# Kernel tuning notes

Measured on AMD Instinct MI355X. Metric: run time of the kernel, lower is better.

## Reference

```python
import jax, jax.numpy as jnp
import numpy as np

NUM_STEPS = 32
THRESHOLD = 1.0
SLOPE = 25.0  # snntorch fast_sigmoid default slope

@jax.custom_vjp
def spike_fn(x):
    # Heaviside forward, fast-sigmoid surrogate backward
    return (x > 0).astype(x.dtype)

def _spike_fwd(x):
    return spike_fn(x), x

def _spike_bwd(x, g):
    return (g / (SLOPE * jnp.abs(x) + 1.0) ** 2,)

spike_fn.defvjp(_spike_fwd, _spike_bwd)


def setup_inputs() -> dict:
    key = jax.random.key(0)
    ks = jax.random.split(key, 4)
    B, F, H, O = 2048, 768, 1024, 16
    def w(k, shape, fan_in):
        return jax.random.normal(k, shape, jnp.float32) / np.float32(np.sqrt(fan_in))
    return {
        "fused": jax.random.normal(ks[0], (B, F), jnp.float32),
        "W_in": w(ks[1], (F, H), F),
        "b_in": jnp.zeros((H,), jnp.float32),
        "W_rec": w(ks[2], (H, H), H),
        "b_rec": jnp.zeros((H,), jnp.float32),
        "W_out": w(ks[3], (H, O), H),
        "b_out": jnp.zeros((O,), jnp.float32),
        "resonant_decay": jnp.full((H,), 0.6, jnp.float32),
        "resonant_frequency": jnp.full((H,), 0.2, jnp.float32),
    }


def reference(fused, W_in, b_in, W_rec, b_rec, W_out, b_out,
              resonant_decay, resonant_frequency):
    # base_current = fusion_in(fused): [B, H]
    base = fused @ W_in + b_in
    decay = 0.55 + 0.4 * jax.nn.sigmoid(resonant_decay)       # [H]
    freq = 0.1 + 0.9 * jax.nn.sigmoid(resonant_frequency)     # [H]
    z = jnp.zeros_like(base)

    def step(carry, _):
        membrane, resonance, recurrent_current = carry
        drive = base + recurrent_current
        resonance = decay * resonance + freq * membrane
        membrane = decay * membrane + drive - resonance
        spikes = spike_fn(membrane - THRESHOLD)
        membrane = membrane - spikes * THRESHOLD
        recurrent_current = spikes @ W_rec + b_rec
        return (membrane, resonance, recurrent_current), spikes

    _, spike_trace = jax.lax.scan(step, (z, z, z), None, length=NUM_STEPS)
    # spike_trace: [T, B, H] (torch stacks on dim=1, mean over time is identical)
    pooled = spike_trace.mean(axis=0)                          # [B, H]
    output = pooled @ W_out + b_out                            # [B, O]
    return output
```

## Files before the change

### kernel.cpp

```cpp
#include <hip/hip_runtime.h>

typedef __attribute__((ext_vector_type(4))) float f32x4;
typedef __attribute__((ext_vector_type(4))) int   i32x4;
typedef __attribute__((ext_vector_type(8))) short s16x8;

#define MFMA16(a, b, c)  __builtin_amdgcn_mfma_f32_16x16x32_bf16((a), (b), (c), 0, 0, 0)
#define MFMAI8(a, b, c)  __builtin_amdgcn_mfma_i32_16x16x64_i8((a), (b), (c), 0, 0, 0)

#define QINV (1.0f / 252.0f)

typedef __attribute__((address_space(3))) unsigned int lds_uint;
typedef const __attribute__((address_space(1))) unsigned int glob_uint;
__device__ __forceinline__ void glds16(const void* g, void* l) {
    __builtin_amdgcn_global_load_lds((glob_uint*)g, (lds_uint*)l, 16, 0, 0);
}

#define SBARL()                                                                \
    {                                                                          \
        __builtin_amdgcn_sched_barrier(0);                                     \
        asm volatile("s_waitcnt lgkmcnt(0)" ::: "memory");                     \
        __builtin_amdgcn_s_barrier();                                          \
        __builtin_amdgcn_sched_barrier(0);                                     \
    }
#define SBAR()                                                                 \
    {                                                                          \
        __builtin_amdgcn_sched_barrier(0);                                     \
        __builtin_amdgcn_s_barrier();                                          \
        __builtin_amdgcn_sched_barrier(0);                                     \
    }

__device__ inline unsigned short f2bf(float f) {
    unsigned int u = __float_as_uint(f);
    return (unsigned short)((u + 0x7FFFu + ((u >> 16) & 1u)) >> 16);
}
__device__ inline float bf2f(unsigned short b) {
    return __uint_as_float(((unsigned int)b) << 16);
}

__global__ __launch_bounds__(256) void k_pack3(const float* __restrict__ W,
                                               unsigned short* __restrict__ L1,
                                               unsigned short* __restrict__ L2,
                                               unsigned short* __restrict__ L3,
                                               int K) {
    int idx = blockIdx.x * 256 + threadIdx.x;
    if (idx >= K * 1024) return;
    int k = idx >> 10;
    int n = idx & 1023;
    float x = W[idx];
    unsigned short h1 = f2bf(x);  float r1 = x - bf2f(h1);
    unsigned short h2 = f2bf(r1); float r2 = r1 - bf2f(h2);
    unsigned short h3 = f2bf(r2);
    size_t o = ((size_t)(k >> 5) << 15) + ((size_t)n << 5) + (k & 31);
    L1[o] = h1; L2[o] = h2; L3[o] = h3;
}

__global__ __launch_bounds__(256) void k_colmax(const float* __restrict__ W,
                                                float* __restrict__ t1) {
    __shared__ float red[256];
    int n = blockIdx.x;
    float m = 0.f;
    for (int k = threadIdx.x; k < 1024; k += 256)
        m = fmaxf(m, fabsf(W[(size_t)k * 1024 + n]));
    red[threadIdx.x] = m;
    __syncthreads();
    for (int s = 128; s > 0; s >>= 1) {
        if (threadIdx.x < s) red[threadIdx.x] = fmaxf(red[threadIdx.x], red[threadIdx.x + s]);
        __syncthreads();
    }
    if (threadIdx.x == 0) t1[n] = fmaxf(red[0], 1e-30f) * (1.0f / 126.0f);
}

__global__ __launch_bounds__(256) void k_packq(const float* __restrict__ W,
                                               const float* __restrict__ t1a,
                                               signed char* __restrict__ Q) {
    int idx = blockIdx.x * 256 + threadIdx.x;
    int k = idx >> 10;
    int n = idx & 1023;
    float x = W[idx];
    float T1 = t1a[n];
    float T2 = T1 * QINV;
    float T3 = T2 * QINV;
    float q1 = rintf(x / T1);  float r1 = fmaf(-q1, T1, x);
    float q2 = rintf(r1 / T2); float r2 = fmaf(-q2, T2, r1);
    float q3 = rintf(r2 / T3);
    int kt = k >> 6, cg = n >> 4;
    int lane = (((k >> 4) & 3) << 4) | (n & 15);
    size_t base = ((size_t)((kt * 64 + cg) * 3)) << 10;
    size_t lj = (size_t)lane * 16 + (k & 15);
    Q[base + lj]        = (signed char)(int)q1;
    Q[base + 1024 + lj] = (signed char)(int)q2;
    Q[base + 2048 + lj] = (signed char)(int)q3;
}

#define FSTR 770
#define LDS_SPK    0
#define LDS_DEC    32768
#define LDS_FRQ    33792
#define LDS_T1     34816
#define LDS_RING   35840
#define LDS_FUSED  35840
#define LDS_PLDS   35840
#define LDS_TOTAL  134400

#define RING_NT(P, nt, BSRC)                                                   \
    {                                                                          \
        asm volatile("s_waitcnt vmcnt(9)" ::: "memory");                       \
        __builtin_amdgcn_sched_barrier(0);                                     \
        const char* sl = ring + (P) + (nt) * 3072;                             \
        i32x4 Bv0 = *(const i32x4*)(sl + lane16);                              \
        i32x4 Bv1 = *(const i32x4*)(sl + 1024 + lane16);                       \
        i32x4 Bv2 = *(const i32x4*)(sl + 2048 + lane16);                       \
        acc[0][nt][0] = MFMAI8(Af0, Bv0, acc[0][nt][0]);                       \
        acc[1][nt][0] = MFMAI8(Af1, Bv0, acc[1][nt][0]);                       \
        acc[0][nt][1] = MFMAI8(Af0, Bv1, acc[0][nt][1]);                       \
        acc[1][nt][1] = MFMAI8(Af1, Bv1, acc[1][nt][1]);                       \
        acc[0][nt][2] = MFMAI8(Af0, Bv2, acc[0][nt][2]);                       \
        acc[1][nt][2] = MFMAI8(Af1, Bv2, acc[1][nt][2]);                       \
        __builtin_amdgcn_sched_barrier(0);                                     \
        glds16((BSRC),        (void*)sl);                                      \
        glds16((BSRC) + 1024, (void*)(sl + 1024));                             \
        glds16((BSRC) + 2048, (void*)(sl + 2048));                             \
    }
#define RING_NTL(P, nt, N)                                                     \
    {                                                                          \
        asm volatile("s_waitcnt vmcnt(" #N ")" ::: "memory");                  \
        __builtin_amdgcn_sched_barrier(0);                                     \
        const char* sl = ring + (P) + (nt) * 3072;                             \
        i32x4 Bv0 = *(const i32x4*)(sl + lane16);                              \
        i32x4 Bv1 = *(const i32x4*)(sl + 1024 + lane16);                       \
        i32x4 Bv2 = *(const i32x4*)(sl + 2048 + lane16);                       \
        acc[0][nt][0] = MFMAI8(Af0, Bv0, acc[0][nt][0]);                       \
        acc[1][nt][0] = MFMAI8(Af1, Bv0, acc[1][nt][0]);                       \
        acc[0][nt][1] = MFMAI8(Af0, Bv1, acc[0][nt][1]);                       \
        acc[1][nt][1] = MFMAI8(Af1, Bv1, acc[1][nt][1]);                       \
        acc[0][nt][2] = MFMAI8(Af0, Bv2, acc[0][nt][2]);                       \
        acc[1][nt][2] = MFMAI8(Af1, Bv2, acc[1][nt][2]);                       \
    }

__global__ __launch_bounds__(512, 2) void k_main(const float* __restrict__ fused,
                                                 const unsigned short* __restrict__ Wi1,
                                                 const unsigned short* __restrict__ Wi2,
                                                 const unsigned short* __restrict__ Wi3,
                                                 const float* __restrict__ b_in,
                                                 const signed char* __restrict__ WrQ,
                                                 const float* __restrict__ t1a,
                                                 const float* __restrict__ b_rec,
                                                 const float* __restrict__ rdec,
                                                 const float* __restrict__ rfrq,
                                                 const float* __restrict__ W_out,
                                                 const float* __restrict__ b_out,
                                                 char* __restrict__ sx,
                                                 unsigned long long* __restrict__ pdb,
                                                 unsigned int* __restrict__ flags,
                                                 float* __restrict__ out) {
    extern __shared__ __align__(16) char smem[];
    const int tid = threadIdx.x;
    const int w = tid >> 6, lane = tid & 63;
    const int llo = lane & 15, lhi = lane >> 4;
    const int bid = blockIdx.x;
    const int q = bid >> 2, h = bid & 3;
    const int r0 = q * 32;
    const int cbase = h * 256;
    const int cg0 = h * 16 + w * 2;
    const int lane16 = lane * 16;
    const int ax = (llo & 7) << 4;

    float* fl = (float*)(smem + LDS_FUSED);
    for (int i = tid; i < 32 * 768; i += 512) {
        int rr = i / 768, cc = i - rr * 768;
        fl[rr * FSTR + cc] = fused[(size_t)(r0 + rr) * 768 + cc];
    }
    __syncthreads();

    f32x4 bacc[2][2] = {};
    for (int kt = 0; kt < 24; ++kt) {
        s16x8 a1v[2], a2v[2], a3v[2];
#pragma unroll
        for (int m = 0; m < 2; ++m) {
            const float* ap = fl + (m * 16 + llo) * FSTR + kt * 32 + lhi * 8;
#pragma unroll
            for (int j = 0; j < 8; ++j) {
                float x = ap[j];
                unsigned short h1 = f2bf(x);  float r1 = x - bf2f(h1);
                unsigned short h2 = f2bf(r1); float r2 = r1 - bf2f(h2);
                a1v[m][j] = (short)h1; a2v[m][j] = (short)h2; a3v[m][j] = (short)f2bf(r2);
            }
        }
#pragma unroll
        for (int nt = 0; nt < 2; ++nt) {
            int c = cbase + w * 32 + nt * 16 + llo;
            size_t boff = ((size_t)(kt * 1024 + c) << 5) + lhi * 8;
            s16x8 b1 = *(const s16x8*)&Wi1[boff];
            s16x8 b2 = *(const s16x8*)&Wi2[boff];
            s16x8 b3 = *(const s16x8*)&Wi3[boff];
#pragma unroll
            for (int m = 0; m < 2; ++m) {
                bacc[m][nt] = MFMA16(a1v[m], b1, bacc[m][nt]);
                bacc[m][nt] = MFMA16(a1v[m], b2, bacc[m][nt]);
                bacc[m][nt] = MFMA16(a2v[m], b1, bacc[m][nt]);
                bacc[m][nt] = MFMA16(a2v[m], b2, bacc[m][nt]);
                bacc[m][nt] = MFMA16(a1v[m], b3, bacc[m][nt]);
                bacc[m][nt] = MFMA16(a3v[m], b1, bacc[m][nt]);
            }
        }
    }
    __syncthreads();

    float* ldsDec = (float*)(smem + LDS_DEC);
    float* ldsFrq = (float*)(smem + LDS_FRQ);
    float* ldsT1  = (float*)(smem + LDS_T1);
    if (tid < 256) {
        int c = cbase + tid;
        ldsDec[tid] = (float)(0.55 + 0.4 / (1.0 + exp(-(double)rdec[c])));
        ldsFrq[tid] = (float)(0.10 + 0.9 / (1.0 + exp(-(double)rfrq[c])));
        ldsT1[tid]  = t1a[c];
    }

    float base2[2][2][4];
    float mem[2][2][4], res[2][2][4];
    unsigned int pooled_pk[4] = {0, 0, 0, 0};
    char* ring = smem + LDS_RING + w * 12288;
    unsigned long long myb = 0;
#pragma unroll
    for (int m = 0; m < 2; ++m)
#pragma unroll
        for (int nt = 0; nt < 2; ++nt) {
            int c = cbase + w * 32 + nt * 16 + llo;
            float bb = b_in[c];
            float brv = b_rec[c];
#pragma unroll
            for (int fr = 0; fr < 4; ++fr) {
                int row = m * 16 + lhi * 4 + fr;
                float b0 = __fadd_rn(bacc[m][nt][fr], bb);
                base2[m][nt][fr] = __fadd_rn(b0, brv);
                float m_ = __fadd_rn(0.f, b0);
                int s = (m_ > 1.0f) ? 1 : 0;
                res[m][nt][fr] = 0.f;
                mem[m][nt][fr] = __fadd_rn(m_, -(float)s);
                pooled_pk[m * 2 + nt] += (unsigned int)s << (8 * fr);
                unsigned long long b = __ballot(s);
                myb = (lane == (m * 8 + nt * 4 + fr)) ? b : myb;
                *(unsigned char*)(smem + ((row * 1024 + c) ^ ((row & 7) << 4))) =
                    (unsigned char)s;
            }
        }
    if (lane < 16)
        __hip_atomic_store((unsigned long long*)(sx + q * 4096 + h * 1024 + w * 128 + lane * 8),
                           myb, __ATOMIC_RELAXED, __HIP_MEMORY_SCOPE_AGENT);
    __builtin_amdgcn_sched_barrier(0);
    {
#pragma unroll
        for (int kk = 0; kk < 2; ++kk)
#pragma unroll
            for (int nt = 0; nt < 2; ++nt) {
                const signed char* b =
                    WrQ + (((size_t)(((4 * h + kk) * 64 + cg0 + nt) * 3)) << 10) + lane16;
                char* sl = ring + kk * 6144 + nt * 3072;
                glds16(b,        (void*)sl);
                glds16(b + 1024, (void*)(sl + 1024));
                glds16(b + 2048, (void*)(sl + 2048));
            }
    }
    __builtin_amdgcn_sched_barrier(0);
    asm volatile("s_waitcnt vmcnt(12)" ::: "memory");
    SBARL();
    if (tid == 0)
        __hip_atomic_store(&flags[q * 4 + h], 1u,
                           __ATOMIC_RELAXED, __HIP_MEMORY_SCOPE_AGENT);

    for (int t = 1; t < 32; ++t) {
        i32x4 acc[2][2][3] = {};

#pragma unroll
        for (int i = 0; i < 4; ++i) {
            const int kt = 4 * h + i;
            const int P = (i & 1) * 6144;
            i32x4 Af0 = *(const i32x4*)(smem + ((llo * 1024 + kt * 64 + lhi * 16) ^ ax));
            i32x4 Af1 = *(const i32x4*)(smem + (((16 + llo) * 1024 + kt * 64 + lhi * 16) ^ ax));
            const int nkt = (kt + 2) & 15;
            const signed char* b0 = WrQ + (((size_t)((nkt * 64 + cg0) * 3)) << 10) + lane16;
            const signed char* b1 = WrQ + (((size_t)((nkt * 64 + cg0 + 1) * 3)) << 10) + lane16;
            RING_NT(P, 0, b0)
            RING_NT(P, 1, b1)
        }

        if (tid < 4 && tid != h) {
            while (__hip_atomic_load(&flags[(t - 1) * 256 + q * 4 + tid],
                                     __ATOMIC_ACQUIRE, __HIP_MEMORY_SCOPE_AGENT) == 0)
                __builtin_amdgcn_s_sleep(2);
        }
        SBAR();
        if (tid < 384) {
            int hh = tid >> 7;
            int hsrc = hh + (hh >= h ? 1 : 0);
            int inner = tid & 127;
            unsigned long long B = __hip_atomic_load(
                (unsigned long long*)(sx + (((t - 1) & 1) * 262144) + q * 4096
                                      + hsrc * 1024 + inner * 8),
                __ATOMIC_RELAXED, __HIP_MEMORY_SCOPE_AGENT);
            int l = inner & 15, wsrc = inner >> 4;
            int fr = l & 3, nt = (l >> 2) & 1, m = (l >> 3) & 1;
            int colb = hsrc * 256 + wsrc * 32 + nt * 16;
#pragma unroll
            for (int l2 = 0; l2 < 4; ++l2) {
                int row = m * 16 + l2 * 4 + fr;
                unsigned int b16 = (unsigned int)(B >> (l2 * 16)) & 0xFFFFu;
                i32x4 v;
#pragma unroll
                for (int qq = 0; qq < 4; ++qq) {
                    unsigned int b4 = (b16 >> (qq * 4)) & 0xFu;
                    v[qq] = (int)((b4 & 1u) | ((b4 >> 1) & 1u) << 8 |
                                  ((b4 >> 2) & 1u) << 16 | ((b4 >> 3) & 1u) << 24);
                }
                *(i32x4*)(smem + ((row * 1024 + colb) ^ ((row & 7) << 4))) = v;
            }
        }
        SBARL();

#pragma unroll 2
        for (int i = 4; i < 14; ++i) {
            const int kt = (4 * h + i) & 15;
            const int P = (i & 1) * 6144;
            i32x4 Af0 = *(const i32x4*)(smem + ((llo * 1024 + kt * 64 + lhi * 16) ^ ax));
            i32x4 Af1 = *(const i32x4*)(smem + (((16 + llo) * 1024 + kt * 64 + lhi * 16) ^ ax));
            const int nkt = (4 * h + i + 2) & 15;
            const signed char* b0 = WrQ + (((size_t)((nkt * 64 + cg0) * 3)) << 10) + lane16;
            const signed char* b1 = WrQ + (((size_t)((nkt * 64 + cg0 + 1) * 3)) << 10) + lane16;
            RING_NT(P, 0, b0)
            RING_NT(P, 1, b1)
        }
        {
            const int kt = (4 * h + 14) & 15;
            i32x4 Af0 = *(const i32x4*)(smem + ((llo * 1024 + kt * 64 + lhi * 16) ^ ax));
            i32x4 Af1 = *(const i32x4*)(smem + (((16 + llo) * 1024 + kt * 64 + lhi * 16) ^ ax));
            RING_NTL(0, 0, 9) RING_NTL(0, 1, 6)
        }
        {
            const int kt = (4 * h + 15) & 15;
            i32x4 Af0 = *(const i32x4*)(smem + ((llo * 1024 + kt * 64 + lhi * 16) ^ ax));
            i32x4 Af1 = *(const i32x4*)(smem + (((16 + llo) * 1024 + kt * 64 + lhi * 16) ^ ax));
            RING_NTL(6144, 0, 3) RING_NTL(6144, 1, 0)
        }

        myb = 0;
#pragma unroll
        for (int m = 0; m < 2; ++m)
#pragma unroll
            for (int nt = 0; nt < 2; ++nt) {
                int lc = w * 32 + nt * 16 + llo;
                int c = cbase + lc;
                float dcc = ldsDec[lc], fqc = ldsFrq[lc], t1c = ldsT1[lc];
#pragma unroll
                for (int fr = 0; fr < 4; ++fr) {
                    int row = m * 16 + lhi * 4 + fr;
                    float s3 = (float)acc[m][nt][2][fr];
                    float s2 = fmaf(s3, QINV, (float)acc[m][nt][1][fr]);
                    float rec = __fmul_rn(fmaf(s2, QINV, (float)acc[m][nt][0][fr]), t1c);
                    float drive = __fadd_rn(base2[m][nt][fr], rec);
                    float rnew = __fadd_rn(__fmul_rn(dcc, res[m][nt][fr]),
                                           __fmul_rn(fqc, mem[m][nt][fr]));
                    float tt = __fadd_rn(__fmul_rn(dcc, mem[m][nt][fr]), drive);
                    float m_ = __fadd_rn(tt, -rnew);
                    int s = (m_ > 1.0f) ? 1 : 0;
                    res[m][nt][fr] = rnew;
                    mem[m][nt][fr] = __fadd_rn(m_, -(float)s);
                    pooled_pk[m * 2 + nt] += (unsigned int)s << (8 * fr);
                    unsigned long long b = __ballot(s);
                    myb = (lane == (m * 8 + nt * 4 + fr)) ? b : myb;
                    if (t < 31)
                        *(unsigned char*)(smem + ((row * 1024 + c) ^ ((row & 7) << 4))) =
                            (unsigned char)s;
                }
            }
        if (t < 31) {
            if (lane < 16)
                __hip_atomic_store((unsigned long long*)(sx + ((t & 1) * 262144) + q * 4096
                                                         + h * 1024 + w * 128 + lane * 8),
                                   myb, __ATOMIC_RELAXED, __HIP_MEMORY_SCOPE_AGENT);
            __builtin_amdgcn_sched_barrier(0);
#pragma unroll
            for (int kk = 0; kk < 2; ++kk)
#pragma unroll
                for (int nt = 0; nt < 2; ++nt) {
                    const signed char* b =
                        WrQ + (((size_t)(((4 * h + kk) * 64 + cg0 + nt) * 3)) << 10) + lane16;
                    char* sl = ring + kk * 6144 + nt * 3072;
                    glds16(b,        (void*)sl);
                    glds16(b + 1024, (void*)(sl + 1024));
                    glds16(b + 2048, (void*)(sl + 2048));
                }
            __builtin_amdgcn_sched_barrier(0);
            asm volatile("s_waitcnt vmcnt(12)" ::: "memory");
            SBARL();
            if (tid == 0)
                __hip_atomic_store(&flags[t * 256 + q * 4 + h], 1u,
                                   __ATOMIC_RELAXED, __HIP_MEMORY_SCOPE_AGENT);
        }
    }

    __syncthreads();
    float* plds = (float*)(smem + LDS_PLDS);
#pragma unroll
    for (int m = 0; m < 2; ++m)
#pragma unroll
        for (int nt = 0; nt < 2; ++nt) {
            int lc = w * 32 + nt * 16 + llo;
#pragma unroll
            for (int fr = 0; fr < 4; ++fr)
                plds[(m * 16 + lhi * 4 + fr) * 264 + lc] =
                    (float)((pooled_pk[m * 2 + nt] >> (8 * fr)) & 255u) * 0.03125f;
        }
    __syncthreads();
    double part = 0.0;
    {
        int row = tid >> 4, o = tid & 15;
        for (int j = 0; j < 256; ++j)
            part += (double)plds[row * 264 + j] * (double)W_out[(size_t)(cbase + j) * 16 + o];
    }
    if (h != 0) {
        __hip_atomic_store(&pdb[(q * 4 + h) * 512 + tid], __double_as_longlong(part),
                           __ATOMIC_RELAXED, __HIP_MEMORY_SCOPE_AGENT);
        __syncthreads();
        if (tid == 0)
            __hip_atomic_store(&flags[32 * 256 + q * 4 + h], 1u,
                               __ATOMIC_RELEASE, __HIP_MEMORY_SCOPE_AGENT);
    } else {
        if (tid == 0) {
#pragma unroll
            for (int hp = 1; hp < 4; ++hp)
                while (__hip_atomic_load(&flags[32 * 256 + q * 4 + hp],
                                         __ATOMIC_ACQUIRE, __HIP_MEMORY_SCOPE_AGENT) == 0)
                    __builtin_amdgcn_s_sleep(2);
        }
        __syncthreads();
        {
            int row = tid >> 4, o = tid & 15;
            double tot = part;
#pragma unroll
            for (int hp = 1; hp < 4; ++hp) {
                unsigned long long pb = __hip_atomic_load(&pdb[(q * 4 + hp) * 512 + tid],
                                                          __ATOMIC_RELAXED,
                                                          __HIP_MEMORY_SCOPE_AGENT);
                tot += __longlong_as_double(pb);
            }
            out[(size_t)(r0 + row) * 16 + o] = __fadd_rn((float)tot, b_out[o]);
        }
    }
}

extern "C" void kernel_launch(void* const* d_in, const int* in_sizes, int n_in,
                              void* d_out, int out_size, void* d_ws, size_t ws_size,
                              hipStream_t stream) {
    const float* fused = (const float*)d_in[0];
    const float* W_in  = (const float*)d_in[1];
    const float* b_in  = (const float*)d_in[2];
    const float* W_rec = (const float*)d_in[3];
    const float* b_rec = (const float*)d_in[4];
    const float* W_out = (const float*)d_in[5];
    const float* b_out = (const float*)d_in[6];
    const float* rdec  = (const float*)d_in[7];
    const float* rfrq  = (const float*)d_in[8];

    char* ws = (char*)d_ws;
    signed char*        WrQ   = (signed char*)(ws);
    float*              t1a   = (float*)(ws + 3145728);
    unsigned short*     Wi1   = (unsigned short*)(ws + 3407872);
    unsigned short*     Wi2   = (unsigned short*)(ws + 4980736);
    unsigned short*     Wi3   = (unsigned short*)(ws + 6553600);
    char*               sx    = ws + 8126464;
    unsigned long long* pdb   = (unsigned long long*)(ws + 8650752);
    unsigned int*       flags = (unsigned int*)(ws + 9699328);
    float* out = (float*)d_out;

    hipFuncSetAttribute((const void*)k_main,
                        hipFuncAttributeMaxDynamicSharedMemorySize, LDS_TOTAL);

    hipMemsetAsync(flags, 0, 33 * 256 * 4, stream);
    hipLaunchKernelGGL(k_colmax, dim3(1024), dim3(256), 0, stream, W_rec, t1a);
    hipLaunchKernelGGL(k_packq, dim3(4096), dim3(256), 0, stream, W_rec, t1a, WrQ);
    hipLaunchKernelGGL(k_pack3, dim3(3072), dim3(256), 0, stream, W_in, Wi1, Wi2, Wi3, 768);

    void* args[] = {(void*)&fused, (void*)&Wi1, (void*)&Wi2, (void*)&Wi3, (void*)&b_in,
                    (void*)&WrQ, (void*)&t1a, (void*)&b_rec, (void*)&rdec, (void*)&rfrq,
                    (void*)&W_out, (void*)&b_out, (void*)&sx, (void*)&pdb, (void*)&flags,
                    (void*)&out};
    hipLaunchCooperativeKernel((void*)k_main, dim3(256), dim3(512), args, LDS_TOTAL, stream);
}
```

Baseline: 444.9 us.

## Overlap per-thread flag polling with MFMA work and coalesce column-max reduction

The main loop no longer has a single thread per source poll the flags followed by a block barrier. Each of the 384 loader threads now spins on its own source's flag and loads the spike bits right away, with two of the four local k-tiles of MFMA work placed between the poll and the unpack so the wait overlaps compute. Separately, the column-max prepass now reads W_rec row-coalesced across 128 blocks and merges results with an integer atomicMax. That needs an extra memset, and packq now writes the final scale. The trade is many more spinning threads and extra atomics in exchange for removing one barrier and the strided loads.

```diff
diff --git a/kernel.cpp b/kernel.cpp
--- a/kernel.cpp
+++ b/kernel.cpp
@@ -19,12 +19,6 @@
     {                                                                          \
         __builtin_amdgcn_sched_barrier(0);                                     \
         asm volatile("s_waitcnt lgkmcnt(0)" ::: "memory");                     \
-        __builtin_amdgcn_s_barrier();                                          \
-        __builtin_amdgcn_sched_barrier(0);                                     \
-    }
-#define SBAR()                                                                 \
-    {                                                                          \
-        __builtin_amdgcn_sched_barrier(0);                                     \
         __builtin_amdgcn_s_barrier();                                          \
         __builtin_amdgcn_sched_barrier(0);                                     \
     }
@@ -55,29 +49,29 @@
 }
 
 __global__ __launch_bounds__(256) void k_colmax(const float* __restrict__ W,
-                                                float* __restrict__ t1) {
-    __shared__ float red[256];
-    int n = blockIdx.x;
-    float m = 0.f;
-    for (int k = threadIdx.x; k < 1024; k += 256)
-        m = fmaxf(m, fabsf(W[(size_t)k * 1024 + n]));
-    red[threadIdx.x] = m;
-    __syncthreads();
-    for (int s = 128; s > 0; s >>= 1) {
-        if (threadIdx.x < s) red[threadIdx.x] = fmaxf(red[threadIdx.x], red[threadIdx.x + s]);
-        __syncthreads();
-    }
-    if (threadIdx.x == 0) t1[n] = fmaxf(red[0], 1e-30f) * (1.0f / 126.0f);
+                                                unsigned int* __restrict__ t1u) {
+    __shared__ float cmax[1024];
+    for (int i = threadIdx.x; i < 1024; i += 256) cmax[i] = 0.f;
+    __syncthreads();
+    int k0 = blockIdx.x * 8;
+    for (int r = 0; r < 8; ++r)
+        for (int c = threadIdx.x; c < 1024; c += 256)
+            cmax[c] = fmaxf(cmax[c], fabsf(W[(size_t)(k0 + r) * 1024 + c]));
+    __syncthreads();
+    for (int c = threadIdx.x; c < 1024; c += 256)
+        atomicMax(&t1u[c], __float_as_uint(cmax[c]));
 }
 
 __global__ __launch_bounds__(256) void k_packq(const float* __restrict__ W,
-                                               const float* __restrict__ t1a,
+                                               const unsigned int* __restrict__ t1u,
+                                               float* __restrict__ t1a,
                                                signed char* __restrict__ Q) {
     int idx = blockIdx.x * 256 + threadIdx.x;
     int k = idx >> 10;
     int n = idx & 1023;
     float x = W[idx];
-    float T1 = t1a[n];
+    float T1 = fmaxf(__uint_as_float(t1u[n]), 1e-30f) * (1.0f / 126.0f);
+    if (k == 0) t1a[n] = T1;
     float T2 = T1 * QINV;
     float T3 = T2 * QINV;
     float q1 = rintf(x / T1);  float r1 = fmaf(-q1, T1, x);
@@ -272,7 +266,7 @@
         i32x4 acc[2][2][3] = {};
 
 #pragma unroll
-        for (int i = 0; i < 4; ++i) {
+        for (int i = 0; i < 2; ++i) {
             const int kt = 4 * h + i;
             const int P = (i & 1) * 6144;
             i32x4 Af0 = *(const i32x4*)(smem + ((llo * 1024 + kt * 64 + lhi * 16) ^ ax));
@@ -284,27 +278,42 @@
             RING_NT(P, 1, b1)
         }
 
-        if (tid < 4 && tid != h) {
-            while (__hip_atomic_load(&flags[(t - 1) * 256 + q * 4 + tid],
+        unsigned long long Bbits = 0;
+        int hsrc_t = 0, inner_t = 0;
+        if (tid < 384) {
+            int hh = tid >> 7;
+            hsrc_t = hh + (hh >= h ? 1 : 0);
+            inner_t = tid & 127;
+            while (__hip_atomic_load(&flags[(t - 1) * 256 + q * 4 + hsrc_t],
                                      __ATOMIC_ACQUIRE, __HIP_MEMORY_SCOPE_AGENT) == 0)
                 __builtin_amdgcn_s_sleep(2);
-        }
-        SBAR();
+            Bbits = __hip_atomic_load(
+                (unsigned long long*)(sx + (((t - 1) & 1) * 262144) + q * 4096
+                                      + hsrc_t * 1024 + inner_t * 8),
+                __ATOMIC_RELAXED, __HIP_MEMORY_SCOPE_AGENT);
+        }
+
+#pragma unroll
+        for (int i = 2; i < 4; ++i) {
+            const int kt = 4 * h + i;
+            const int P = (i & 1) * 6144;
+            i32x4 Af0 = *(const i32x4*)(smem + ((llo * 1024 + kt * 64 + lhi * 16) ^ ax));
+            i32x4 Af1 = *(const i32x4*)(smem + (((16 + llo) * 1024 + kt * 64 + lhi * 16) ^ ax));
+            const int nkt = (kt + 2) & 15;
+            const signed char* b0 = WrQ + (((size_t)((nkt * 64 + cg0) * 3)) << 10) + lane16;
+            const signed char* b1 = WrQ + (((size_t)((nkt * 64 + cg0 + 1) * 3)) << 10) + lane16;
+            RING_NT(P, 0, b0)
+            RING_NT(P, 1, b1)
+        }
+
         if (tid < 384) {
-            int hh = tid >> 7;
-            int hsrc = hh + (hh >= h ? 1 : 0);
-            int inner = tid & 127;
-            unsigned long long B = __hip_atomic_load(
-                (unsigned long long*)(sx + (((t - 1) & 1) * 262144) + q * 4096
-                                      + hsrc * 1024 + inner * 8),
-                __ATOMIC_RELAXED, __HIP_MEMORY_SCOPE_AGENT);
-            int l = inner & 15, wsrc = inner >> 4;
+            int l = inner_t & 15, wsrc = inner_t >> 4;
             int fr = l & 3, nt = (l >> 2) & 1, m = (l >> 3) & 1;
-            int colb = hsrc * 256 + wsrc * 32 + nt * 16;
+            int colb = hsrc_t * 256 + wsrc * 32 + nt * 16;
 #pragma unroll
             for (int l2 = 0; l2 < 4; ++l2) {
                 int row = m * 16 + l2 * 4 + fr;
-                unsigned int b16 = (unsigned int)(B >> (l2 * 16)) & 0xFFFFu;
+                unsigned int b16 = (unsigned int)(Bbits >> (l2 * 16)) & 0xFFFFu;
                 i32x4 v;
 #pragma unroll
                 for (int qq = 0; qq < 4; ++qq) {
@@ -464,6 +473,7 @@
     char* ws = (char*)d_ws;
     signed char*        WrQ   = (signed char*)(ws);
     float*              t1a   = (float*)(ws + 3145728);
+    unsigned int*       t1u   = (unsigned int*)(ws + 3149824);
     unsigned short*     Wi1   = (unsigned short*)(ws + 3407872);
     unsigned short*     Wi2   = (unsigned short*)(ws + 4980736);
     unsigned short*     Wi3   = (unsigned short*)(ws + 6553600);
@@ -476,8 +486,9 @@
                         hipFuncAttributeMaxDynamicSharedMemorySize, LDS_TOTAL);
 
     hipMemsetAsync(flags, 0, 33 * 256 * 4, stream);
-    hipLaunchKernelGGL(k_colmax, dim3(1024), dim3(256), 0, stream, W_rec, t1a);
-    hipLaunchKernelGGL(k_packq, dim3(4096), dim3(256), 0, stream, W_rec, t1a, WrQ);
+    hipMemsetAsync(t1u, 0, 4096, stream);
+    hipLaunchKernelGGL(k_colmax, dim3(128), dim3(256), 0, stream, W_rec, t1u);
+    hipLaunchKernelGGL(k_packq, dim3(4096), dim3(256), 0, stream, W_rec, t1u, t1a, WrQ);
     hipLaunchKernelGGL(k_pack3, dim3(3072), dim3(256), 0, stream, W_in, Wi1, Wi2, Wi3, 768);
 
     void* args[] = {(void*)&fused, (void*)&Wi1, (void*)&Wi2, (void*)&Wi3, (void*)&b_in,
```

New measurement: 753.7 us. 1.69x slower.
